# Kernel tuning notes

Measured on AMD Instinct MI355X. Metric: run time of the kernel, lower is better.

The kernel has to match this reference:

```python
import jax, jax.numpy as jnp
import numpy as np

N_DOC, N_WORD = 20000, 80000
N = N_DOC + N_WORD
E = 1_000_000
HID = 64
M = 10000


def setup_inputs() -> dict:
    key = jax.random.key(0)
    ks = jax.random.split(key, 10)
    doc_features = jax.random.normal(ks[0], (N_DOC, 768), dtype=jnp.float32)
    word_features = jax.random.normal(ks[1], (N_WORD, 300), dtype=jnp.float32)
    edge_index = jax.random.randint(ks[2], (2, E), 0, N, dtype=jnp.int64)
    edge_weight = jax.random.uniform(ks[3], (E,), dtype=jnp.float32)
    mask_idx = jax.random.randint(ks[4], (M,), 0, N, dtype=jnp.int64)
    y = jax.random.randint(ks[5], (N,), 0, 4, dtype=jnp.int64)
    s = 0.02
    W_lin = jax.random.normal(ks[6], (300, 768), dtype=jnp.float32) * s
    b_lin = jnp.zeros((768,), dtype=jnp.float32)
    W1 = jax.random.normal(ks[7], (768, HID), dtype=jnp.float32) * s
    b1 = jnp.zeros((HID,), dtype=jnp.float32)
    W2 = jax.random.normal(ks[8], (HID, HID), dtype=jnp.float32) * s
    b2 = jnp.zeros((HID,), dtype=jnp.float32)
    return {"doc_features": doc_features, "word_features": word_features,
            "edge_weight": edge_weight, "W_lin": W_lin, "b_lin": b_lin,
            "W1": W1, "b1": b1, "W2": W2, "b2": b2,
            "edge_index": edge_index, "mask_idx": mask_idx, "y": y}


def _gcn_norm(edge_index, edge_weight, num_nodes):
    # PyG gcn_norm: add self loops (weight 1), symmetric normalization.
    row, col = edge_index[0], edge_index[1]
    loop = jnp.arange(num_nodes, dtype=row.dtype)
    row = jnp.concatenate([row, loop])
    col = jnp.concatenate([col, loop])
    w = jnp.concatenate([edge_weight, jnp.ones((num_nodes,), edge_weight.dtype)])
    deg = jax.ops.segment_sum(w, col, num_segments=num_nodes)
    dis = jnp.where(deg > 0, jax.lax.rsqrt(jnp.maximum(deg, 1e-12)), 0.0)
    norm = dis[row] * w * dis[col]
    return row, col, norm


def _gcn_layer(x, W, b, row, col, norm, num_nodes):
    xw = x @ W                              # [N, out]
    msg = xw[row] * norm[:, None]           # gather + weight  [E+N, out]
    out = jax.ops.segment_sum(msg, col, num_segments=num_nodes)  # scatter-add
    return out + b


def reference(doc_features, word_features, edge_weight, W_lin, b_lin,
              W1, b1, W2, b2, edge_index, mask_idx, y):
    word = word_features @ W_lin + b_lin            # [N_WORD, 768]
    x = jnp.concatenate([doc_features, word], axis=0)  # [N, 768]
    num_nodes = x.shape[0]
    row, col, norm = _gcn_norm(edge_index, edge_weight, num_nodes)
    x = _gcn_layer(x, W1, b1, row, col, norm, num_nodes)
    x = jax.nn.relu(x)
    # dropout is identity in eval mode
    x = _gcn_layer(x, W2, b2, row, col, norm, num_nodes)
    return x[mask_idx], y[mask_idx]
```

## Files before the change

### kernel.cpp

```cpp
#include <hip/hip_runtime.h>


typedef __attribute__((ext_vector_type(8))) short short8;
typedef __attribute__((ext_vector_type(4))) float float4v;

__device__ __forceinline__ unsigned short f2bf(float f) {
  unsigned u = __float_as_uint(f);
  return (unsigned short)((u + 0x7FFFu + ((u >> 16) & 1u)) >> 16);
}
__device__ __forceinline__ float bf2f(unsigned short u) {
  return __uint_as_float((unsigned)u << 16);
}
__device__ __forceinline__ int permcol(int p) {
  return ((p & 3) << 4) | (p >> 2);
}

template <bool PERM>
__device__ __forceinline__ void pack_w_body(const float* __restrict__ W, int K,
                                            int nk0, unsigned short* __restrict__ pack,
                                            int tid) {
  int lane = tid & 63;
  int rest = tid >> 6;
  int k0 = rest % nk0;
  int g = rest / nk0;
  int quad = lane >> 4;
  int n = (lane & 15) + g * 16;
  short8 v;
#pragma unroll
  for (int j = 0; j < 8; ++j) {
    int k = k0 * 32 + quad * 8 + j;
    int ks = PERM ? permcol(k) : k;
    float w = (k < K) ? W[(size_t)ks * 64 + n] : 0.f;
    v[j] = (short)f2bf(w);
  }
  *(short8*)(pack + (((size_t)(g * nk0 + k0) * 64 + lane) << 3)) = v;
}

template <bool LAST, bool BF16PERM, int NK0, int CHUNK>
__device__ __forceinline__ void mfma_gemm_body(
    const float* __restrict__ X, int ldx, const float* __restrict__ lastRow,
    const unsigned short* __restrict__ Wpack,
    int K, const float* __restrict__ bias,
    void* __restrict__ outv, int R, int waveIdx) {
  int r0 = waveIdx * 16;
  if (r0 >= R) return;
  const int lane = threadIdx.x & 63;
  const int quad = lane >> 4;
  const int m = lane & 15;
  const float* xrow = nullptr;
  {
    int row = r0 + m;
    if (row < R) xrow = (LAST && row == R - 1) ? lastRow : X + (size_t)row * ldx;
  }

  float4v acc[4];
#pragma unroll
  for (int g = 0; g < 4; ++g) acc[g] = (float4v){0.f, 0.f, 0.f, 0.f};

#pragma unroll
  for (int c0 = 0; c0 < NK0; c0 += CHUNK) {
    float a[CHUNK][8];
#pragma unroll
    for (int cc = 0; cc < CHUNK; ++cc) {
      int kb = (c0 + cc) * 32 + quad * 8;
      if (xrow && kb + 8 <= K) {
        float4 v0 = *(const float4*)(xrow + kb);
        float4 v1 = *(const float4*)(xrow + kb + 4);
        a[cc][0] = v0.x; a[cc][1] = v0.y; a[cc][2] = v0.z; a[cc][3] = v0.w;
        a[cc][4] = v1.x; a[cc][5] = v1.y; a[cc][6] = v1.z; a[cc][7] = v1.w;
      } else {
#pragma unroll
        for (int j = 0; j < 8; ++j) {
          int k = kb + j;
          a[cc][j] = (xrow && k < K) ? xrow[k] : 0.f;
        }
      }
    }
#pragma unroll
    for (int cc = 0; cc < CHUNK; ++cc) {
      int k0 = c0 + cc;
      short8 bf[4];
#pragma unroll
      for (int g = 0; g < 4; ++g)
        bf[g] = *(const short8*)(Wpack + (((size_t)(g * NK0 + k0) * 64 + lane) << 3));
      short8 af;
#pragma unroll
      for (int j = 0; j < 8; ++j) af[j] = (short)f2bf(a[cc][j]);
#pragma unroll
      for (int g = 0; g < 4; ++g)
        acc[g] = __builtin_amdgcn_mfma_f32_16x16x32_bf16(af, bf[g], acc[g], 0, 0, 0);
    }
  }

  if (BF16PERM) {
    float b0 = bias ? bias[m] : 0.f;
    float b1 = bias ? bias[16 + m] : 0.f;
    float b2 = bias ? bias[32 + m] : 0.f;
    float b3 = bias ? bias[48 + m] : 0.f;
#pragma unroll
    for (int j = 0; j < 4; ++j) {
      int r = r0 + quad * 4 + j;
      if (r < R) {
        ushort4 pk;
        pk.x = f2bf(acc[0][j] + b0);
        pk.y = f2bf(acc[1][j] + b1);
        pk.z = f2bf(acc[2][j] + b2);
        pk.w = f2bf(acc[3][j] + b3);
        *(ushort4*)((unsigned short*)outv + ((size_t)r * 64 + m * 4)) = pk;
      }
    }
  } else {
#pragma unroll
    for (int g = 0; g < 4; ++g) {
      float b = bias ? bias[g * 16 + m] : 0.f;
#pragma unroll
      for (int reg = 0; reg < 4; ++reg) {
        int r = r0 + quad * 4 + reg;
        if (r < R) ((float*)outv)[(size_t)r * 64 + g * 16 + m] = acc[g][reg] + b;
      }
    }
  }
}

__global__ __launch_bounds__(256) void k_pack(
    const float* __restrict__ W1, unsigned short* __restrict__ packW1,
    const float* __restrict__ W2, unsigned short* __restrict__ packW2) {
  int b = blockIdx.x;
  int t = threadIdx.x;
  if (b < 24) { pack_w_body<false>(W1, 768, 24, packW1, b * 256 + t); return; }
  b -= 24;
  pack_w_body<true>(W2, 64, 2, packW2, b * 256 + t);
}

__global__ __launch_bounds__(256) void k_pre(
    const float* __restrict__ Wlin, const float* __restrict__ blin,
    const unsigned short* __restrict__ packW1, float* __restrict__ WfuseB,
    int histBlocks,
    const int* __restrict__ ei, int E, int* __restrict__ bucketTot, int nbuck) {
  int b = blockIdx.x;
  int t = threadIdx.x;
  if (b < histBlocks) {
    __shared__ int h[512];
    h[t] = 0; h[t + 256] = 0;
    __syncthreads();
    int e0 = b * 4096;
#pragma unroll 4
    for (int i = 0; i < 16; ++i) {
      int e = e0 + t + i * 256;
      if (e < E) atomicAdd(&h[ei[E + e] >> 8], 1);
    }
    __syncthreads();
    if (t < nbuck && h[t]) atomicAdd(bucketTot + t, h[t]);
    if (t + 256 < nbuck && h[t + 256]) atomicAdd(bucketTot + t + 256, h[t + 256]);
    return;
  }
  b -= histBlocks;
  mfma_gemm_body<true, false, 24, 8>(Wlin, 768, blin, packW1, 768,
                                     nullptr, WfuseB, 301, b * 4 + (t >> 6));
}

__global__ __launch_bounds__(512) void k_scanB(
    const int* __restrict__ bucketTot, int nbuck,
    int* __restrict__ bucketBase, int* __restrict__ bucketRun,
    const float* __restrict__ WfuseB, unsigned short* __restrict__ packWf) {
  int t = threadIdx.x;
  if (blockIdx.x > 0) {
    pack_w_body<false>(WfuseB, 300, 10, packWf, ((int)blockIdx.x - 1) * 512 + t);
    return;
  }
  __shared__ int s[512];
  int v = (t < nbuck) ? bucketTot[t] : 0;
  s[t] = v; __syncthreads();
  for (int off = 1; off < 512; off <<= 1) {
    int x = (t >= off) ? s[t - off] : 0;
    __syncthreads();
    s[t] += x;
    __syncthreads();
  }
  if (t < nbuck) {
    int ex = s[t] - v;
    bucketBase[t] = ex;
    bucketRun[t] = ex;
  }
  if (t == nbuck - 1) bucketBase[nbuck] = s[t];
}

__global__ __launch_bounds__(256) void k_sd(
    const int* __restrict__ ei, const float* __restrict__ ew, int E,
    int scatBlocks, int* __restrict__ bucketRun, int2* __restrict__ ebuf,
    const float* __restrict__ doc, const unsigned short* __restrict__ packW1,
    unsigned short* __restrict__ xw1, int ND) {
  int b = blockIdx.x;
  int t = threadIdx.x;
  if (b >= scatBlocks) {
    mfma_gemm_body<false, true, 24, 8>(doc, 768, nullptr, packW1, 768,
                                       nullptr, xw1, ND, (b - scatBlocks) * 4 + (t >> 6));
    return;
  }
  __shared__ int h[512];
  __shared__ int base[512];
  __shared__ int cur[512];
  h[t] = 0; h[t + 256] = 0;
  __syncthreads();
  int e0 = b * 4096;
#pragma unroll 4
  for (int i = 0; i < 16; ++i) {
    int e = e0 + t + i * 256;
    if (e < E) atomicAdd(&h[ei[E + e] >> 8], 1);
  }
  __syncthreads();
#pragma unroll
  for (int k = t; k < 512; k += 256) {
    if (h[k]) base[k] = atomicAdd(bucketRun + k, h[k]);
    cur[k] = 0;
  }
  __syncthreads();
#pragma unroll 4
  for (int i = 0; i < 16; ++i) {
    int e = e0 + t + i * 256;
    if (e < E) {
      int d = ei[E + e];
      int bk = d >> 8;
      int r = base[bk] + atomicAdd(&cur[bk], 1);
      ebuf[r] = make_int2(ei[e] | ((d & 255) << 17), __float_as_int(ew[e]));
    }
  }
}

__global__ __launch_bounds__(256) void k_bw(
    const int2* __restrict__ ebuf, const int* __restrict__ bucketBase,
    int nbuck, int N, int* __restrict__ offs, float* __restrict__ dis,
    int2* __restrict__ entries,
    const float* __restrict__ wordf, const unsigned short* __restrict__ packWf,
    const float* __restrict__ bfuse, unsigned short* __restrict__ xw1word, int NW) {
  int b = blockIdx.x;
  int t = threadIdx.x;
  if (b >= nbuck) {
    mfma_gemm_body<false, true, 10, 5>(wordf, 300, nullptr, packWf, 300,
                                       bfuse, xw1word, NW, (b - nbuck) * 4 + (t >> 6));
    return;
  }
  __shared__ int scnt[256];
  __shared__ float swd[256];
  __shared__ int sscan[256];
  __shared__ int scur[256];
  int node0 = b << 8;
  int nn = min(256, N - node0);
  int estart = bucketBase[b], eend = bucketBase[b + 1];
  scnt[t] = (t < nn) ? 1 : 0;
  swd[t] = (t < nn) ? 1.f : 0.f;
  __syncthreads();
  for (int p = estart + t; p < eend; p += 256) {
    int2 e = ebuf[p];
    int low = (e.x >> 17) & 255;
    atomicAdd(&scnt[low], 1);
    atomicAdd(&swd[low], __int_as_float(e.y));
  }
  __syncthreads();
  int v = scnt[t];
  sscan[t] = v; __syncthreads();
  for (int off = 1; off < 256; off <<= 1) {
    int x = (t >= off) ? sscan[t - off] : 0;
    __syncthreads();
    sscan[t] += x;
    __syncthreads();
  }
  int excl = sscan[t] - v;
  int entriesBase = estart + node0;
  if (t < nn) {
    offs[node0 + t] = entriesBase + excl;
    dis[node0 + t] = rsqrtf(fmaxf(swd[t], 1e-12f));
    entries[entriesBase + excl] = make_int2(node0 + t, __float_as_int(1.0f));
  }
  scur[t] = excl + 1;
  if (t == 0 && b == nbuck - 1) offs[N] = entriesBase + (eend - estart) + nn;
  __syncthreads();
  for (int p = estart + t; p < eend; p += 256) {
    int2 e = ebuf[p];
    int low = (e.x >> 17) & 255;
    int r = atomicAdd(&scur[low], 1);
    entries[entriesBase + r] = make_int2(e.x & 0x1FFFF, e.y);
  }
}

__device__ __forceinline__ void row_gather2(const unsigned short* __restrict__ xin,
                                            const int2* __restrict__ entries,
                                            const float* __restrict__ dis,
                                            int p, int pe, int l32,
                                            float& ra0, float& ra1) {
  float a0 = 0.f, a1 = 0.f;
  for (; p + 8 <= pe; p += 8) {
    int2 e[8];
#pragma unroll
    for (int j = 0; j < 8; ++j) e[j] = entries[p + j];
    unsigned x[8];
    float ds[8];
#pragma unroll
    for (int j = 0; j < 8; ++j) {
      x[j] = *(const unsigned*)(xin + ((size_t)e[j].x << 6) + (l32 << 1));
      ds[j] = dis[e[j].x];
    }
#pragma unroll
    for (int j = 0; j < 8; ++j) {
      float w = __int_as_float(e[j].y) * ds[j];
      a0 = fmaf(bf2f((unsigned short)(x[j] & 0xffffu)), w, a0);
      a1 = fmaf(bf2f((unsigned short)(x[j] >> 16)), w, a1);
    }
  }
  if (p + 4 <= pe) {
    int2 e[4];
#pragma unroll
    for (int j = 0; j < 4; ++j) e[j] = entries[p + j];
    unsigned x[4];
    float ds[4];
#pragma unroll
    for (int j = 0; j < 4; ++j) {
      x[j] = *(const unsigned*)(xin + ((size_t)e[j].x << 6) + (l32 << 1));
      ds[j] = dis[e[j].x];
    }
#pragma unroll
    for (int j = 0; j < 4; ++j) {
      float w = __int_as_float(e[j].y) * ds[j];
      a0 = fmaf(bf2f((unsigned short)(x[j] & 0xffffu)), w, a0);
      a1 = fmaf(bf2f((unsigned short)(x[j] >> 16)), w, a1);
    }
    p += 4;
  }
  for (; p < pe; ++p) {
    int2 e = entries[p];
    unsigned x = *(const unsigned*)(xin + ((size_t)e.x << 6) + (l32 << 1));
    float w = __int_as_float(e.y) * dis[e.x];
    a0 = fmaf(bf2f((unsigned short)(x & 0xffffu)), w, a0);
    a1 = fmaf(bf2f((unsigned short)(x >> 16)), w, a1);
  }
  ra0 = a0; ra1 = a1;
}

__global__ void k_agg(const unsigned short* __restrict__ xin, const int2* __restrict__ entries,
                      const int* __restrict__ offs, const float* __restrict__ dis,
                      const float* __restrict__ bias, unsigned short* __restrict__ xout, int N) {
  const int tid = threadIdx.x;
  const int l32 = tid & 31;
  int i = blockIdx.x * 8 + (tid >> 5);
  if (i >= N) return;
  float a0, a1;
  row_gather2(xin, entries, dis, offs[i], offs[i + 1], l32, a0, a1);
  float d = dis[i];
  a0 = fmaxf(fmaf(a0, d, bias[permcol(2 * l32)]), 0.f);
  a1 = fmaxf(fmaf(a1, d, bias[permcol(2 * l32 + 1)]), 0.f);
  ushort2 pk;
  pk.x = f2bf(a0);
  pk.y = f2bf(a1);
  *(ushort2*)(xout + ((size_t)i << 6) + (l32 << 1)) = pk;
}

__global__ void k_agg2m(const unsigned short* __restrict__ xin, const int2* __restrict__ entries,
                        const int* __restrict__ offs, const float* __restrict__ dis,
                        const int* __restrict__ mask, const int* __restrict__ y,
                        float* __restrict__ tout, float* __restrict__ outY, int M) {
  const int tid = threadIdx.x;
  const int l32 = tid & 31;
  int o = blockIdx.x * 8 + (tid >> 5);
  if (o >= M) return;
  int i = mask[o];
  float a0, a1;
  row_gather2(xin, entries, dis, offs[i], offs[i + 1], l32, a0, a1);
  float d = dis[i];
  float2 pk;
  pk.x = a0 * d;
  pk.y = a1 * d;
  *(float2*)(tout + ((size_t)o << 6) + (l32 << 1)) = pk;
  if (l32 == 0) outY[o] = (float)y[i];
}

__global__ __launch_bounds__(256) void k_mfma_final(
    const float* __restrict__ X, const unsigned short* __restrict__ packW2,
    const float* __restrict__ b2, float* __restrict__ out, int M) {
  mfma_gemm_body<false, false, 2, 2>(X, 64, nullptr, packW2, 64,
                                     b2, out, M, blockIdx.x * 4 + (threadIdx.x >> 6));
}

extern "C" void kernel_launch(void* const* d_in, const int* in_sizes, int n_in,
                              void* d_out, int out_size, void* d_ws, size_t ws_size,
                              hipStream_t stream) {
  const float* doc   = (const float*)d_in[0];
  const float* wordf = (const float*)d_in[1];
  const float* ew    = (const float*)d_in[2];
  const float* Wlin  = (const float*)d_in[3];
  const float* blin  = (const float*)d_in[4];
  const float* W1    = (const float*)d_in[5];
  const float* b1    = (const float*)d_in[6];
  const float* W2    = (const float*)d_in[7];
  const float* b2    = (const float*)d_in[8];
  const int*   ei    = (const int*)d_in[9];
  const int*   mask  = (const int*)d_in[10];
  const int*   y     = (const int*)d_in[11];

  const int E  = in_sizes[2];
  const int M  = in_sizes[10];
  const int ND = in_sizes[0] / 768;
  const int NW = in_sizes[1] / 300;
  const int N  = ND + NW;
  const int NE = N + E;
  const int nbuck = (N + 255) >> 8;

  char* p = (char*)d_ws;
  auto carve = [&](size_t bytes) -> void* {
    void* q = (void*)p;
    p += (bytes + 255) & ~(size_t)255;
    return q;
  };
  float*          WfuseB = (float*)carve(301 * 64 * 4);
  unsigned short* packW1 = (unsigned short*)carve((size_t)4 * 24 * 64 * 8 * 2);
  unsigned short* packW2 = (unsigned short*)carve((size_t)4 * 2 * 64 * 8 * 2);
  unsigned short* packWf = (unsigned short*)carve((size_t)4 * 10 * 64 * 8 * 2);
  float* dis       = (float*)carve((size_t)N * 4);
  int*   offs      = (int*)carve(((size_t)N + 1) * 4);
  int*   bucketTot = (int*)carve((size_t)(nbuck + 2) * 4);
  int*   bucketBase= (int*)carve((size_t)(nbuck + 2) * 4);
  int*   bucketRun = (int*)carve((size_t)(nbuck + 2) * 4);
  int2*  ebuf      = (int2*)carve((size_t)E * 8);
  int2*  entries   = (int2*)carve((size_t)NE * 8);
  unsigned short* xw1 = (unsigned short*)carve((size_t)N * 64 * 2);
  unsigned short* h1  = (unsigned short*)carve((size_t)N * 64 * 2);
  float* tmask = (float*)carve((size_t)M * 64 * 4);

  hipMemsetAsync(bucketTot, 0, (size_t)nbuck * 4, stream);

  k_pack<<<26, 256, 0, stream>>>(W1, packW1, W2, packW2);

  const int fuseBlocks = (301 + 63) / 64;
  const int histBlocks = (E + 4095) / 4096;
  k_pre<<<histBlocks + fuseBlocks, 256, 0, stream>>>(
      Wlin, blin, packW1, WfuseB, histBlocks, ei, E, bucketTot, nbuck);

  k_scanB<<<6, 512, 0, stream>>>(bucketTot, nbuck, bucketBase, bucketRun,
                                 WfuseB, packWf);

  const int docBlocks  = (ND + 63) / 64;
  k_sd<<<histBlocks + docBlocks, 256, 0, stream>>>(
      ei, ew, E, histBlocks, bucketRun, ebuf,
      doc, packW1, xw1, ND);

  const int wordBlocks = (NW + 63) / 64;
  k_bw<<<nbuck + wordBlocks, 256, 0, stream>>>(
      ebuf, bucketBase, nbuck, N, offs, dis, entries,
      wordf, packWf, WfuseB + (size_t)300 * 64, xw1 + (size_t)ND * 64, NW);

  k_agg<<<(N + 7) / 8, 256, 0, stream>>>(xw1, entries, offs, dis, b1, h1, N);

  float* out0 = (float*)d_out;
  float* outY = out0 + (size_t)M * 64;
  k_agg2m<<<(M + 7) / 8, 256, 0, stream>>>(h1, entries, offs, dis, mask, y, tmask, outY, M);
  k_mfma_final<<<(M + 63) / 64, 256, 0, stream>>>(tmask, packW2, b2, out0, M);
}
```

Before: 327.7 us.

## Rebalance GEMM work across graph-preprocessing kernels and fold memset into pack

Moves the doc-feature GEMM into the histogram kernel k_pre, and splits the word-feature GEMM between the scatter kernel k_sd and the bucket-build kernel k_bw so each launch carries a more even mix of work. The bucket-counter memset is replaced by an extra block in the pack kernel, which removes one separate API operation. The goal is to overlap the dense GEMMs with the latency-bound edge-sorting stages and cut idle gaps between launches. The trade-off is that k_pre becomes heavier and the critical path may shift.

```diff
diff --git a/kernel.cpp b/kernel.cpp
--- a/kernel.cpp
+++ b/kernel.cpp
@@ -124,19 +124,22 @@
 
 __global__ __launch_bounds__(256) void k_pack(
     const float* __restrict__ W1, unsigned short* __restrict__ packW1,
-    const float* __restrict__ W2, unsigned short* __restrict__ packW2) {
+    const float* __restrict__ W2, unsigned short* __restrict__ packW2,
+    int* __restrict__ bucketTot, int nbuck) {
   int b = blockIdx.x;
   int t = threadIdx.x;
   if (b < 24) { pack_w_body<false>(W1, 768, 24, packW1, b * 256 + t); return; }
   b -= 24;
-  pack_w_body<true>(W2, 64, 2, packW2, b * 256 + t);
+  if (b < 2) { pack_w_body<true>(W2, 64, 2, packW2, b * 256 + t); return; }
+  for (int i = t; i < nbuck + 2; i += 256) bucketTot[i] = 0;
 }
 
 __global__ __launch_bounds__(256) void k_pre(
     const float* __restrict__ Wlin, const float* __restrict__ blin,
     const unsigned short* __restrict__ packW1, float* __restrict__ WfuseB,
-    int histBlocks,
-    const int* __restrict__ ei, int E, int* __restrict__ bucketTot, int nbuck) {
+    int histBlocks, int fuseBlocks,
+    const int* __restrict__ ei, int E, int* __restrict__ bucketTot, int nbuck,
+    const float* __restrict__ doc, unsigned short* __restrict__ xw1, int ND) {
   int b = blockIdx.x;
   int t = threadIdx.x;
   if (b < histBlocks) {
@@ -155,8 +158,14 @@
     return;
   }
   b -= histBlocks;
-  mfma_gemm_body<true, false, 24, 8>(Wlin, 768, blin, packW1, 768,
-                                     nullptr, WfuseB, 301, b * 4 + (t >> 6));
+  if (b < fuseBlocks) {
+    mfma_gemm_body<true, false, 24, 8>(Wlin, 768, blin, packW1, 768,
+                                       nullptr, WfuseB, 301, b * 4 + (t >> 6));
+    return;
+  }
+  b -= fuseBlocks;
+  mfma_gemm_body<false, true, 24, 8>(doc, 768, nullptr, packW1, 768,
+                                     nullptr, xw1, ND, b * 4 + (t >> 6));
 }
 
 __global__ __launch_bounds__(512) void k_scanB(
@@ -188,13 +197,13 @@
 __global__ __launch_bounds__(256) void k_sd(
     const int* __restrict__ ei, const float* __restrict__ ew, int E,
     int scatBlocks, int* __restrict__ bucketRun, int2* __restrict__ ebuf,
-    const float* __restrict__ doc, const unsigned short* __restrict__ packW1,
-    unsigned short* __restrict__ xw1, int ND) {
+    const float* __restrict__ wordf, const unsigned short* __restrict__ packWf,
+    const float* __restrict__ bfuse, unsigned short* __restrict__ xw1word, int NWsd) {
   int b = blockIdx.x;
   int t = threadIdx.x;
   if (b >= scatBlocks) {
-    mfma_gemm_body<false, true, 24, 8>(doc, 768, nullptr, packW1, 768,
-                                       nullptr, xw1, ND, (b - scatBlocks) * 4 + (t >> 6));
+    mfma_gemm_body<false, true, 10, 5>(wordf, 300, nullptr, packWf, 300,
+                                       bfuse, xw1word, NWsd, (b - scatBlocks) * 4 + (t >> 6));
     return;
   }
   __shared__ int h[512];
@@ -231,13 +240,13 @@
     const int2* __restrict__ ebuf, const int* __restrict__ bucketBase,
     int nbuck, int N, int* __restrict__ offs, float* __restrict__ dis,
     int2* __restrict__ entries,
-    const float* __restrict__ wordf, const unsigned short* __restrict__ packWf,
-    const float* __restrict__ bfuse, unsigned short* __restrict__ xw1word, int NW) {
+    const float* __restrict__ wordf2, const unsigned short* __restrict__ packWf,
+    const float* __restrict__ bfuse, unsigned short* __restrict__ xw1word2, int NW2) {
   int b = blockIdx.x;
   int t = threadIdx.x;
   if (b >= nbuck) {
-    mfma_gemm_body<false, true, 10, 5>(wordf, 300, nullptr, packWf, 300,
-                                       bfuse, xw1word, NW, (b - nbuck) * 4 + (t >> 6));
+    mfma_gemm_body<false, true, 10, 5>(wordf2, 300, nullptr, packWf, 300,
+                                       bfuse, xw1word2, NW2, (b - nbuck) * 4 + (t >> 6));
     return;
   }
   __shared__ int scnt[256];
@@ -425,27 +434,32 @@
   unsigned short* h1  = (unsigned short*)carve((size_t)N * 64 * 2);
   float* tmask = (float*)carve((size_t)M * 64 * 4);
 
-  hipMemsetAsync(bucketTot, 0, (size_t)nbuck * 4, stream);
-
-  k_pack<<<26, 256, 0, stream>>>(W1, packW1, W2, packW2);
+  k_pack<<<27, 256, 0, stream>>>(W1, packW1, W2, packW2, bucketTot, nbuck);
 
   const int fuseBlocks = (301 + 63) / 64;
+  const int docBlocks  = (ND + 63) / 64;
   const int histBlocks = (E + 4095) / 4096;
-  k_pre<<<histBlocks + fuseBlocks, 256, 0, stream>>>(
-      Wlin, blin, packW1, WfuseB, histBlocks, ei, E, bucketTot, nbuck);
+  k_pre<<<histBlocks + fuseBlocks + docBlocks, 256, 0, stream>>>(
+      Wlin, blin, packW1, WfuseB, histBlocks, fuseBlocks,
+      ei, E, bucketTot, nbuck, doc, xw1, ND);
 
   k_scanB<<<6, 512, 0, stream>>>(bucketTot, nbuck, bucketBase, bucketRun,
                                  WfuseB, packWf);
 
-  const int docBlocks  = (ND + 63) / 64;
-  k_sd<<<histBlocks + docBlocks, 256, 0, stream>>>(
+  const int wordBlocks = (NW + 63) / 64;
+  const int wsdBlocks  = wordBlocks / 2;
+  const int wsdRows    = wsdBlocks * 64;
+  unsigned short* xw1word = xw1 + (size_t)ND * 64;
+  const float*    bfuse   = WfuseB + (size_t)300 * 64;
+
+  k_sd<<<histBlocks + wsdBlocks, 256, 0, stream>>>(
       ei, ew, E, histBlocks, bucketRun, ebuf,
-      doc, packW1, xw1, ND);
-
-  const int wordBlocks = (NW + 63) / 64;
-  k_bw<<<nbuck + wordBlocks, 256, 0, stream>>>(
+      wordf, packWf, bfuse, xw1word, wsdRows);
+
+  k_bw<<<nbuck + (wordBlocks - wsdBlocks), 256, 0, stream>>>(
       ebuf, bucketBase, nbuck, N, offs, dis, entries,
-      wordf, packWf, WfuseB + (size_t)300 * 64, xw1 + (size_t)ND * 64, NW);
+      wordf + (size_t)wsdRows * 300, packWf, bfuse,
+      xw1word + (size_t)wsdRows * 64, NW - wsdRows);
 
   k_agg<<<(N + 7) / 8, 256, 0, stream>>>(xw1, entries, offs, dis, b1, h1, N);
 
```

After: 317.6 us. -3.1%, faster.
